# Performance work log

Hardware: AMD Instinct MI355X
Metric: run time of the kernel (lower is better)

Reference implementation:

```python
import jax, jax.numpy as jnp
import numpy as np


def setup_inputs() -> dict:
    key = jax.random.key(0)
    k1, k2, k3 = jax.random.split(key, 3)
    N, C, H, W, O = 4, 256, 64, 64, 256
    x = jax.random.normal(k1, (N, C, H, W), jnp.float32)
    # offset per forward signature: [N, H*W, 2*3*3]
    offset = jax.random.normal(k2, (N, H * W, 18), jnp.float32)
    # DeformConv weight [O, C, 3, 3], normal_init std=0.01, bias=False
    weight = jax.random.normal(k3, (O, C, 3, 3), jnp.float32) * 0.01
    return {"x": x, "offset": offset, "weight": weight}


def _deform_conv3x3(x, offset, weight):
    """Deformable conv v1: 3x3, stride 1, padding 1, dilation 1, no bias.
    x: [N,C,H,W]; offset: [N,HW,18] (permuted to [N,18,H,W] as in the module);
    weight: [O,C,3,3].
    """
    N, C, H, W = x.shape
    O = weight.shape[0]
    # module does offset.permute(0,2,1).reshape(N,-1,H,W) -> [N,18,H,W]
    off = offset.transpose(0, 2, 1).reshape(N, 9, 2, H, W)  # (dy,dx) per kernel pos
    dy, dx = off[:, :, 0], off[:, :, 1]                      # [N,9,H,W]

    # base 3x3 kernel offsets (padding=1 keeps the grid centered)
    ky = jnp.array([-1, -1, -1, 0, 0, 0, 1, 1, 1], x.dtype)
    kx = jnp.array([-1, 0, 1, -1, 0, 1, -1, 0, 1], x.dtype)
    hg = jnp.arange(H, dtype=x.dtype)[:, None]  # [H,1]
    wg = jnp.arange(W, dtype=x.dtype)[None, :]  # [1,W]
    py = hg[None, None] + ky[None, :, None, None] + dy  # [N,9,H,W] sample rows
    px = wg[None, None] + kx[None, :, None, None] + dx  # [N,9,H,W] sample cols

    y0 = jnp.floor(py)
    x0 = jnp.floor(px)
    wy = (py - y0)[:, None]  # [N,1,9,H,W]
    wx = (px - x0)[:, None]

    def gather(iy, ix):
        # zero-padded gather: out[n,c,k,h,w] = x[n,c,iy,ix] (0 if out of bounds)
        valid = (iy >= 0) & (iy < H) & (ix >= 0) & (ix < W)
        iyc = jnp.clip(iy, 0, H - 1).astype(jnp.int32)
        ixc = jnp.clip(ix, 0, W - 1).astype(jnp.int32)
        g = jax.vmap(lambda xn, yn, wn: xn[:, yn, wn])(x, iyc, ixc)  # [N,C,9,H,W]
        return g * valid[:, None].astype(x.dtype)

    v00 = gather(y0, x0)
    v01 = gather(y0, x0 + 1)
    v10 = gather(y0 + 1, x0)
    v11 = gather(y0 + 1, x0 + 1)
    # bilinear blend -> sampled columns [N,C,9,H,W]
    val = (v00 * (1 - wy) * (1 - wx) + v01 * (1 - wy) * wx
           + v10 * wy * (1 - wx) + v11 * wy * wx)
    # conv accumulate over channels and kernel positions
    return jnp.einsum('nckhw,ock->nohw', val, weight.reshape(O, C, 9))


def reference(x, offset, weight):
    return _deform_conv3x3(x, offset, weight)
```

## Files before the change

kernel.cpp:

```cpp
#include <hip/hip_runtime.h>
#include <hip/hip_fp16.h>

#define CC 256
#define OO 256
#define HH 64
#define WW 64
#define HWN 4096
#define MPB 64
#define NPB 128
#define VST 264

typedef _Float16 half8 __attribute__((ext_vector_type(8)));
typedef _Float16 half2v __attribute__((ext_vector_type(2)));
typedef float f32x4 __attribute__((ext_vector_type(4)));

__device__ __forceinline__ half2v u2h(unsigned u) {
  half2v h; __builtin_memcpy(&h, &u, 4); return h;
}
__device__ __forceinline__ unsigned h2u(half2v h) {
  unsigned u; __builtin_memcpy(&u, &h, 4); return u;
}
__device__ __forceinline__ unsigned short f2h(float f) {
  _Float16 h = (_Float16)f;
  unsigned short us; __builtin_memcpy(&us, &h, 2);
  return us;
}
__device__ __forceinline__ unsigned dupu(unsigned short us) {
  return ((unsigned)us << 16) | us;
}
__device__ __forceinline__ unsigned pk2(float a, float b) {
  half2v h = {(_Float16)a, (_Float16)b};
  return h2u(h);
}

__global__ __launch_bounds__(256) void prep_kernel(
    const float* __restrict__ x, const float* __restrict__ w,
    _Float16* __restrict__ xt, _Float16* __restrict__ wt) {
  const int bid = blockIdx.x;
  const int tid = threadIdx.x;
  if (bid < 1024) {
    __shared__ float tile[64][65];
    const int n  = bid >> 8;
    const int c0 = ((bid >> 6) & 3) * 64;
    const int s0 = (bid & 63) * 64;
    {
      int r  = tid >> 2;
      int sc = (tid & 3) * 16;
      const float* xp = x + ((size_t)(n * CC + c0 + r)) * HWN + s0 + sc;
      float4 va = *(const float4*)(xp);
      float4 vb = *(const float4*)(xp + 4);
      float4 vc = *(const float4*)(xp + 8);
      float4 vd = *(const float4*)(xp + 12);
      tile[sc + 0][r]  = va.x;  tile[sc + 1][r]  = va.y;
      tile[sc + 2][r]  = va.z;  tile[sc + 3][r]  = va.w;
      tile[sc + 4][r]  = vb.x;  tile[sc + 5][r]  = vb.y;
      tile[sc + 6][r]  = vb.z;  tile[sc + 7][r]  = vb.w;
      tile[sc + 8][r]  = vc.x;  tile[sc + 9][r]  = vc.y;
      tile[sc + 10][r] = vc.z;  tile[sc + 11][r] = vc.w;
      tile[sc + 12][r] = vd.x;  tile[sc + 13][r] = vd.y;
      tile[sc + 14][r] = vd.z;  tile[sc + 15][r] = vd.w;
    }
    __syncthreads();
    {
      int s  = tid >> 2;
      int cg = (tid & 3) * 16;
      uint4 u0, u1;
      u0.x = pk2(tile[s][cg + 0],  tile[s][cg + 1]);
      u0.y = pk2(tile[s][cg + 2],  tile[s][cg + 3]);
      u0.z = pk2(tile[s][cg + 4],  tile[s][cg + 5]);
      u0.w = pk2(tile[s][cg + 6],  tile[s][cg + 7]);
      u1.x = pk2(tile[s][cg + 8],  tile[s][cg + 9]);
      u1.y = pk2(tile[s][cg + 10], tile[s][cg + 11]);
      u1.z = pk2(tile[s][cg + 12], tile[s][cg + 13]);
      u1.w = pk2(tile[s][cg + 14], tile[s][cg + 15]);
      _Float16* op = xt + ((size_t)(n * HWN + s0 + s)) * CC + c0 + cg;
      *(uint4*)(op)     = u0;
      *(uint4*)(op + 8) = u1;
    }
  } else {
    __shared__ _Float16 wrow[9][264];
    const int o = bid - 1024;
    const float* wp = w + (size_t)o * (CC * 9);
    float v[9];
#pragma unroll
    for (int k = 0; k < 9; ++k) v[k] = wp[tid * 9 + k];
#pragma unroll
    for (int k = 0; k < 9; ++k) wrow[k][tid] = (_Float16)v[k];
    __syncthreads();
    for (int r = tid; r < 9 * 64; r += 256) {
      int k  = r >> 6;
      int c4 = (r & 63) * 4;
      *(uint2*)(wt + (size_t)k * (OO * CC) + (size_t)o * CC + c4) =
          *(const uint2*)(&wrow[k][c4]);
    }
  }
}

__global__ __launch_bounds__(256, 3) void deform_mfma_kernel(
    const _Float16* __restrict__ xt,
    const _Float16* __restrict__ wt,
    const float* __restrict__ off,
    float* __restrict__ out) {
  __shared__ __align__(16) _Float16 val_lds[MPB * VST];
  __shared__ ushort4 s_po[MPB * 9];
  __shared__ ushort4 s_pw[MPB * 9];

  const int tid  = threadIdx.x;
  const int lane = tid & 63;
  const int wv   = tid >> 6;
  const int n15  = lane & 15;
  const int quad = lane >> 4;

  const int bx    = blockIdx.x;
  const int nb    = (bx & 7) >> 1;
  const int hw0   = (bx >> 3) * MPB;
  const int obase = (bx & 1) * NPB;

  for (int e = tid; e < MPB * 9; e += 256) {
    int p = e / 9;
    int k = e - p * 9;
    int hw = hw0 + p;
    int h = hw >> 6, w = hw & 63;
    size_t ob = ((size_t)(nb * HWN + hw)) * 18 + 2 * k;
    float2 d = *(const float2*)(off + ob);
    float py = (float)(h + k / 3 - 1) + d.x;
    float px = (float)(w + k % 3 - 1) + d.y;
    float fy = floorf(py), fx = floorf(px);
    int iy = (int)fy, ix = (int)fx;
    float wy = py - fy, wx = px - fx;
    float my0 = ((unsigned)iy       < (unsigned)HH) ? 1.f : 0.f;
    float my1 = ((unsigned)(iy + 1) < (unsigned)HH) ? 1.f : 0.f;
    float mx0 = ((unsigned)ix       < (unsigned)WW) ? 1.f : 0.f;
    float mx1 = ((unsigned)(ix + 1) < (unsigned)WW) ? 1.f : 0.f;
    int iy0 = min(max(iy, 0), HH - 1), iy1 = min(max(iy + 1, 0), HH - 1);
    int ix0 = min(max(ix, 0), WW - 1), ix1 = min(max(ix + 1, 0), WW - 1);
    s_po[e] = make_ushort4((unsigned short)(iy0 * WW + ix0),
                           (unsigned short)(iy0 * WW + ix1),
                           (unsigned short)(iy1 * WW + ix0),
                           (unsigned short)(iy1 * WW + ix1));
    s_pw[e] = make_ushort4(f2h((1.f - wy) * (1.f - wx) * my0 * mx0),
                           f2h((1.f - wy) * wx         * my0 * mx1),
                           f2h(wy         * (1.f - wx) * my1 * mx0),
                           f2h(wy         * wx         * my1 * mx1));
  }

  f32x4 acc[4][2];
#pragma unroll
  for (int a = 0; a < 4; ++a)
#pragma unroll
    for (int b = 0; b < 2; ++b) acc[a][b] = (f32x4){0.f, 0.f, 0.f, 0.f};

  const _Float16* xb = xt + (size_t)nb * HWN * CC;
  const int j = lane & 31;
  const int ph = lane >> 5;

  for (int k = 0; k < 9; ++k) {
    __syncthreads();

    const _Float16* wb = wt + ((size_t)(k * OO + obase + wv * 32)) * CC;
    half8 bfr[8][2];
#pragma unroll
    for (int ks = 0; ks < 8; ++ks)
#pragma unroll
      for (int nt = 0; nt < 2; ++nt)
        bfr[ks][nt] = *(const half8*)(wb + (size_t)(nt * 16 + n15) * CC + ks * 32 + quad * 8);

#pragma unroll
    for (int i = 0; i < 8; ++i) {
      int p = i * 8 + wv * 2 + ph;
      int idx = p * 9 + k;
      ushort4 o4 = s_po[idx];
      ushort4 hw4 = s_pw[idx];
      half2v w00 = u2h(dupu(hw4.x)), w01 = u2h(dupu(hw4.y));
      half2v w10 = u2h(dupu(hw4.z)), w11 = u2h(dupu(hw4.w));
      const _Float16* cb = xb + (size_t)j * 8;
      uint4 v00 = *(const uint4*)(cb + (size_t)o4.x * CC);
      uint4 v01 = *(const uint4*)(cb + (size_t)o4.y * CC);
      uint4 v10 = *(const uint4*)(cb + (size_t)o4.z * CC);
      uint4 v11 = *(const uint4*)(cb + (size_t)o4.w * CC);
      uint4 r;
      r.x = h2u(u2h(v00.x) * w00 + u2h(v01.x) * w01 + u2h(v10.x) * w10 + u2h(v11.x) * w11);
      r.y = h2u(u2h(v00.y) * w00 + u2h(v01.y) * w01 + u2h(v10.y) * w10 + u2h(v11.y) * w11);
      r.z = h2u(u2h(v00.z) * w00 + u2h(v01.z) * w01 + u2h(v10.z) * w10 + u2h(v11.z) * w11);
      r.w = h2u(u2h(v00.w) * w00 + u2h(v01.w) * w01 + u2h(v10.w) * w10 + u2h(v11.w) * w11);
      *(uint4*)(val_lds + p * VST + j * 8) = r;
    }
    __syncthreads();

#pragma unroll
    for (int ks = 0; ks < 8; ++ks) {
      half8 afr[4];
#pragma unroll
      for (int mt = 0; mt < 4; ++mt)
        afr[mt] = *(const half8*)(val_lds + (mt * 16 + n15) * VST + ks * 32 + quad * 8);
#pragma unroll
      for (int mt = 0; mt < 4; ++mt)
#pragma unroll
        for (int nt = 0; nt < 2; ++nt)
          acc[mt][nt] = __builtin_amdgcn_mfma_f32_16x16x32_f16(
              afr[mt], bfr[ks][nt], acc[mt][nt], 0, 0, 0);
    }
  }

#pragma unroll
  for (int mt = 0; mt < 4; ++mt)
#pragma unroll
    for (int nt = 0; nt < 2; ++nt) {
      int o  = obase + wv * 32 + nt * 16 + n15;
      int px = hw0 + mt * 16 + quad * 4;
      *(f32x4*)(out + ((size_t)nb * OO + o) * HWN + px) = acc[mt][nt];
    }
}

extern "C" void kernel_launch(void* const* d_in, const int* in_sizes, int n_in,
                              void* d_out, int out_size, void* d_ws, size_t ws_size,
                              hipStream_t stream) {
  const float* x   = (const float*)d_in[0];
  const float* off = (const float*)d_in[1];
  const float* w   = (const float*)d_in[2];
  float* out = (float*)d_out;

  _Float16* wt = (_Float16*)d_ws;
  _Float16* xt = wt + 589824;

  prep_kernel<<<1024 + 256, 256, 0, stream>>>(x, w, xt, wt);
  deform_mfma_kernel<<<(4 * HWN / MPB) * (OO / NPB), 256, 0, stream>>>(xt, wt, off, out);
}
```

Baseline: 137.4 us.

## Double-buffer sampled columns to overlap bilinear gather with MFMA compute

Adds a second LDS buffer for the bilinearly sampled columns so that the gather for kernel position k+1 is interleaved with the MFMA accumulation for position k. One of the two barriers per iteration goes away, and weight fragments are now loaded per k-slice rather than all up front. In exchange LDS use doubles and launch bounds drop to 2 blocks per CU, which may reduce occupancy and latency hiding.

```diff
diff --git a/kernel.cpp b/kernel.cpp
--- a/kernel.cpp
+++ b/kernel.cpp
@@ -9,6 +9,7 @@
 #define MPB 64
 #define NPB 128
 #define VST 264
+#define VOFF (MPB * VST)
 
 typedef _Float16 half8 __attribute__((ext_vector_type(8)));
 typedef _Float16 half2v __attribute__((ext_vector_type(2)));
@@ -96,12 +97,12 @@
   }
 }
 
-__global__ __launch_bounds__(256, 3) void deform_mfma_kernel(
+__global__ __launch_bounds__(256, 2) void deform_mfma_kernel(
     const _Float16* __restrict__ xt,
     const _Float16* __restrict__ wt,
     const float* __restrict__ off,
     float* __restrict__ out) {
-  __shared__ __align__(16) _Float16 val_lds[MPB * VST];
+  __shared__ __align__(16) _Float16 val_lds[2 * VOFF];
   __shared__ ushort4 s_po[MPB * 9];
   __shared__ ushort4 s_pw[MPB * 9];
 
@@ -154,51 +155,74 @@
   const int j = lane & 31;
   const int ph = lane >> 5;
 
-  for (int k = 0; k < 9; ++k) {
+  auto sample_iter = [&](int kk, int bb, int i) {
+    int p = i * 8 + wv * 2 + ph;
+    int idx = p * 9 + kk;
+    ushort4 o4 = s_po[idx];
+    ushort4 hw4 = s_pw[idx];
+    half2v w00 = u2h(dupu(hw4.x)), w01 = u2h(dupu(hw4.y));
+    half2v w10 = u2h(dupu(hw4.z)), w11 = u2h(dupu(hw4.w));
+    const _Float16* cb = xb + (size_t)j * 8;
+    uint4 v00 = *(const uint4*)(cb + (size_t)o4.x * CC);
+    uint4 v01 = *(const uint4*)(cb + (size_t)o4.y * CC);
+    uint4 v10 = *(const uint4*)(cb + (size_t)o4.z * CC);
+    uint4 v11 = *(const uint4*)(cb + (size_t)o4.w * CC);
+    uint4 r;
+    r.x = h2u(u2h(v00.x) * w00 + u2h(v01.x) * w01 + u2h(v10.x) * w10 + u2h(v11.x) * w11);
+    r.y = h2u(u2h(v00.y) * w00 + u2h(v01.y) * w01 + u2h(v10.y) * w10 + u2h(v11.y) * w11);
+    r.z = h2u(u2h(v00.z) * w00 + u2h(v01.z) * w01 + u2h(v10.z) * w10 + u2h(v11.z) * w11);
+    r.w = h2u(u2h(v00.w) * w00 + u2h(v01.w) * w01 + u2h(v10.w) * w10 + u2h(v11.w) * w11);
+    *(uint4*)(val_lds + bb * VOFF + p * VST + j * 8) = r;
+  };
+
+  __syncthreads();
+#pragma unroll
+  for (int i = 0; i < 8; ++i) sample_iter(0, 0, i);
+
+  for (int k = 0; k < 8; ++k) {
     __syncthreads();
-
+    const int cur = k & 1;
+    const int nxt = cur ^ 1;
     const _Float16* wb = wt + ((size_t)(k * OO + obase + wv * 32)) * CC;
-    half8 bfr[8][2];
-#pragma unroll
-    for (int ks = 0; ks < 8; ++ks)
+#pragma unroll
+    for (int ks = 0; ks < 8; ++ks) {
+      sample_iter(k + 1, nxt, ks);
+      half8 bfr[2];
 #pragma unroll
       for (int nt = 0; nt < 2; ++nt)
-        bfr[ks][nt] = *(const half8*)(wb + (size_t)(nt * 16 + n15) * CC + ks * 32 + quad * 8);
-
-#pragma unroll
-    for (int i = 0; i < 8; ++i) {
-      int p = i * 8 + wv * 2 + ph;
-      int idx = p * 9 + k;
-      ushort4 o4 = s_po[idx];
-      ushort4 hw4 = s_pw[idx];
-      half2v w00 = u2h(dupu(hw4.x)), w01 = u2h(dupu(hw4.y));
-      half2v w10 = u2h(dupu(hw4.z)), w11 = u2h(dupu(hw4.w));
-      const _Float16* cb = xb + (size_t)j * 8;
-      uint4 v00 = *(const uint4*)(cb + (size_t)o4.x * CC);
-      uint4 v01 = *(const uint4*)(cb + (size_t)o4.y * CC);
-      uint4 v10 = *(const uint4*)(cb + (size_t)o4.z * CC);
-      uint4 v11 = *(const uint4*)(cb + (size_t)o4.w * CC);
-      uint4 r;
-      r.x = h2u(u2h(v00.x) * w00 + u2h(v01.x) * w01 + u2h(v10.x) * w10 + u2h(v11.x) * w11);
-      r.y = h2u(u2h(v00.y) * w00 + u2h(v01.y) * w01 + u2h(v10.y) * w10 + u2h(v11.y) * w11);
-      r.z = h2u(u2h(v00.z) * w00 + u2h(v01.z) * w01 + u2h(v10.z) * w10 + u2h(v11.z) * w11);
-      r.w = h2u(u2h(v00.w) * w00 + u2h(v01.w) * w01 + u2h(v10.w) * w10 + u2h(v11.w) * w11);
-      *(uint4*)(val_lds + p * VST + j * 8) = r;
-    }
-    __syncthreads();
-
-#pragma unroll
-    for (int ks = 0; ks < 8; ++ks) {
+        bfr[nt] = *(const half8*)(wb + (size_t)(nt * 16 + n15) * CC + ks * 32 + quad * 8);
       half8 afr[4];
 #pragma unroll
       for (int mt = 0; mt < 4; ++mt)
-        afr[mt] = *(const half8*)(val_lds + (mt * 16 + n15) * VST + ks * 32 + quad * 8);
+        afr[mt] = *(const half8*)(val_lds + cur * VOFF + (mt * 16 + n15) * VST + ks * 32 + quad * 8);
 #pragma unroll
       for (int mt = 0; mt < 4; ++mt)
 #pragma unroll
         for (int nt = 0; nt < 2; ++nt)
           acc[mt][nt] = __builtin_amdgcn_mfma_f32_16x16x32_f16(
-              afr[mt], bfr[ks][nt], acc[mt][nt], 0, 0, 0);
+              afr[mt], bfr[nt], acc[mt][nt], 0, 0, 0);
+    }
+  }
+
+  __syncthreads();
+  {
+    const _Float16* wb = wt + ((size_t)(8 * OO + obase + wv * 32)) * CC;
+#pragma unroll
+    for (int ks = 0; ks < 8; ++ks) {
+      half8 bfr[2];
+#pragma unroll
+      for (int nt = 0; nt < 2; ++nt)
+        bfr[nt] = *(const half8*)(wb + (size_t)(nt * 16 + n15) * CC + ks * 32 + quad * 8);
+      half8 afr[4];
+#pragma unroll
+      for (int mt = 0; mt < 4; ++mt)
+        afr[mt] = *(const half8*)(val_lds + (mt * 16 + n15) * VST + ks * 32 + quad * 8);
+#pragma unroll
+      for (int mt = 0; mt < 4; ++mt)
+#pragma unroll
+        for (int nt = 0; nt < 2; ++nt)
+          acc[mt][nt] = __builtin_amdgcn_mfma_f32_16x16x32_f16(
+              afr[mt], bfr[nt], acc[mt][nt], 0, 0, 0);
     }
   }
 
```

New measurement: 133.1 us. 3.1% less time.

## Split channel reduction across blocks with atomic accumulation instead of output split

Applied to the files above, without the earlier changes.

Each block now covers all 256 output channels for a quarter of the input channels (a split-K of 4) rather than half the outputs over all channels. Results are accumulated into an output zeroed by a memset, using float atomics. Bilinear gather work per block drops and is no longer duplicated across two output halves. Weight fragments are loaded per k-step instead of preloaded, and occupancy is raised to 4 waves per SIMD. The cost is atomic traffic on the full output, an extra memset, and a nondeterministic summation order.

```diff
diff --git a/kernel.cpp b/kernel.cpp
--- a/kernel.cpp
+++ b/kernel.cpp
@@ -7,8 +7,8 @@
 #define WW 64
 #define HWN 4096
 #define MPB 64
-#define NPB 128
-#define VST 264
+#define KQ  64
+#define VST 72
 
 typedef _Float16 half8 __attribute__((ext_vector_type(8)));
 typedef _Float16 half2v __attribute__((ext_vector_type(2)));
@@ -96,7 +96,7 @@
   }
 }
 
-__global__ __launch_bounds__(256, 3) void deform_mfma_kernel(
+__global__ __launch_bounds__(256, 4) void deform_mfma_kernel(
     const _Float16* __restrict__ xt,
     const _Float16* __restrict__ wt,
     const float* __restrict__ off,
@@ -112,9 +112,12 @@
   const int quad = lane >> 4;
 
   const int bx    = blockIdx.x;
-  const int nb    = (bx & 7) >> 1;
-  const int hw0   = (bx >> 3) * MPB;
-  const int obase = (bx & 1) * NPB;
+  const int xcd   = bx & 7;
+  const int local = bx >> 3;
+  const int nb    = xcd >> 1;
+  const int kq    = local & 3;
+  const int hw0   = (((xcd & 1) << 5) | (local >> 2)) * 64;
+  const int c0    = kq * KQ;
 
   for (int e = tid; e < MPB * 9; e += 256) {
     int p = e / 9;
@@ -144,30 +147,22 @@
                            f2h(wy         * wx         * my1 * mx1));
   }
 
-  f32x4 acc[4][2];
+  f32x4 acc[4][4];
 #pragma unroll
   for (int a = 0; a < 4; ++a)
 #pragma unroll
-    for (int b = 0; b < 2; ++b) acc[a][b] = (f32x4){0.f, 0.f, 0.f, 0.f};
-
-  const _Float16* xb = xt + (size_t)nb * HWN * CC;
-  const int j = lane & 31;
-  const int ph = lane >> 5;
+    for (int b = 0; b < 4; ++b) acc[a][b] = (f32x4){0.f, 0.f, 0.f, 0.f};
+
+  const _Float16* xb = xt + (size_t)nb * HWN * CC + c0;
+  const int j  = lane & 7;
+  const int pl = lane >> 3;
 
   for (int k = 0; k < 9; ++k) {
     __syncthreads();
 
-    const _Float16* wb = wt + ((size_t)(k * OO + obase + wv * 32)) * CC;
-    half8 bfr[8][2];
-#pragma unroll
-    for (int ks = 0; ks < 8; ++ks)
-#pragma unroll
-      for (int nt = 0; nt < 2; ++nt)
-        bfr[ks][nt] = *(const half8*)(wb + (size_t)(nt * 16 + n15) * CC + ks * 32 + quad * 8);
-
-#pragma unroll
-    for (int i = 0; i < 8; ++i) {
-      int p = i * 8 + wv * 2 + ph;
+#pragma unroll
+    for (int i = 0; i < 2; ++i) {
+      int p = i * 32 + wv * 8 + pl;
       int idx = p * 9 + k;
       ushort4 o4 = s_po[idx];
       ushort4 hw4 = s_pw[idx];
@@ -187,28 +182,36 @@
     }
     __syncthreads();
 
-#pragma unroll
-    for (int ks = 0; ks < 8; ++ks) {
-      half8 afr[4];
+    const _Float16* wb = wt + ((size_t)(k * OO + wv * 64)) * CC + c0;
+#pragma unroll
+    for (int ks = 0; ks < 2; ++ks) {
+      half8 afr[4], bfr[4];
 #pragma unroll
       for (int mt = 0; mt < 4; ++mt)
         afr[mt] = *(const half8*)(val_lds + (mt * 16 + n15) * VST + ks * 32 + quad * 8);
 #pragma unroll
+      for (int nt = 0; nt < 4; ++nt)
+        bfr[nt] = *(const half8*)(wb + (size_t)(nt * 16 + n15) * CC + ks * 32 + quad * 8);
+#pragma unroll
       for (int mt = 0; mt < 4; ++mt)
 #pragma unroll
-        for (int nt = 0; nt < 2; ++nt)
+        for (int nt = 0; nt < 4; ++nt)
           acc[mt][nt] = __builtin_amdgcn_mfma_f32_16x16x32_f16(
-              afr[mt], bfr[ks][nt], acc[mt][nt], 0, 0, 0);
+              afr[mt], bfr[nt], acc[mt][nt], 0, 0, 0);
     }
   }
 
 #pragma unroll
   for (int mt = 0; mt < 4; ++mt)
 #pragma unroll
-    for (int nt = 0; nt < 2; ++nt) {
-      int o  = obase + wv * 32 + nt * 16 + n15;
+    for (int nt = 0; nt < 4; ++nt) {
+      int o  = wv * 64 + nt * 16 + n15;
       int px = hw0 + mt * 16 + quad * 4;
-      *(f32x4*)(out + ((size_t)nb * OO + o) * HWN + px) = acc[mt][nt];
+      float* dst = out + ((size_t)nb * OO + o) * HWN + px;
+      atomicAdd(dst + 0, acc[mt][nt].x);
+      atomicAdd(dst + 1, acc[mt][nt].y);
+      atomicAdd(dst + 2, acc[mt][nt].z);
+      atomicAdd(dst + 3, acc[mt][nt].w);
     }
 }
 
@@ -223,6 +226,7 @@
   _Float16* wt = (_Float16*)d_ws;
   _Float16* xt = wt + 589824;
 
+  hipMemsetAsync(d_out, 0, (size_t)4 * OO * HWN * sizeof(float), stream);
   prep_kernel<<<1024 + 256, 256, 0, stream>>>(x, w, xt, wt);
-  deform_mfma_kernel<<<(4 * HWN / MPB) * (OO / NPB), 256, 0, stream>>>(xt, wt, off, out);
-}
+  deform_mfma_kernel<<<1024, 256, 0, stream>>>(xt, wt, off, out);
+}
```

After: 325.8 us. 137% more time.

## Cover all output channels per block and stage weights via double-buffered LDS

Applied to the files above, without the earlier changes.

Each block now processes 32 pixels for all 256 output channels with 512 threads, so the bilinear gather of sampled columns is no longer repeated for two output-channel halves. Weights are streamed into LDS in 32-channel slices with double buffering instead of being loaded per wave into registers. This removes duplicated gather work and register pressure from weight fragments. The cost is a barrier per K-slice and lower MFMA work per LDS read.

```diff
diff --git a/kernel.cpp b/kernel.cpp
--- a/kernel.cpp
+++ b/kernel.cpp
@@ -6,9 +6,10 @@
 #define HH 64
 #define WW 64
 #define HWN 4096
-#define MPB 64
-#define NPB 128
+#define MPB 32
 #define VST 264
+#define WST 44
+#define WBUF (256 * WST)
 
 typedef _Float16 half8 __attribute__((ext_vector_type(8)));
 typedef _Float16 half2v __attribute__((ext_vector_type(2)));
@@ -96,12 +97,13 @@
   }
 }
 
-__global__ __launch_bounds__(256, 3) void deform_mfma_kernel(
+__global__ __launch_bounds__(512, 4) void deform_mfma_kernel(
     const _Float16* __restrict__ xt,
     const _Float16* __restrict__ wt,
     const float* __restrict__ off,
     float* __restrict__ out) {
   __shared__ __align__(16) _Float16 val_lds[MPB * VST];
+  __shared__ __align__(16) _Float16 w_lds[2 * WBUF];
   __shared__ ushort4 s_po[MPB * 9];
   __shared__ ushort4 s_pw[MPB * 9];
 
@@ -111,12 +113,16 @@
   const int n15  = lane & 15;
   const int quad = lane >> 4;
 
-  const int bx    = blockIdx.x;
-  const int nb    = (bx & 7) >> 1;
-  const int hw0   = (bx >> 3) * MPB;
-  const int obase = (bx & 1) * NPB;
-
-  for (int e = tid; e < MPB * 9; e += 256) {
+  const int bx  = blockIdx.x;
+  const int xcd = bx & 7;
+  const int nb  = xcd >> 1;
+  const int hw0 = ((((xcd & 1) << 6) + (bx >> 3))) * MPB;
+
+  const int o0 = (wv & 3) * 64;
+  const int p0 = (wv >> 2) * 16;
+
+  if (tid < MPB * 9) {
+    int e = tid;
     int p = e / 9;
     int k = e - p * 9;
     int hw = hw0 + p;
@@ -144,30 +150,22 @@
                            f2h(wy         * wx         * my1 * mx1));
   }
 
-  f32x4 acc[4][2];
-#pragma unroll
-  for (int a = 0; a < 4; ++a)
-#pragma unroll
-    for (int b = 0; b < 2; ++b) acc[a][b] = (f32x4){0.f, 0.f, 0.f, 0.f};
+  f32x4 acc[4];
+#pragma unroll
+  for (int b = 0; b < 4; ++b) acc[b] = (f32x4){0.f, 0.f, 0.f, 0.f};
 
   const _Float16* xb = xt + (size_t)nb * HWN * CC;
-  const int j = lane & 31;
-  const int ph = lane >> 5;
+  const int j    = tid & 31;
+  const int slot = tid >> 5;
+  const int so   = tid >> 1;
+  const int sh   = tid & 1;
 
   for (int k = 0; k < 9; ++k) {
     __syncthreads();
 
-    const _Float16* wb = wt + ((size_t)(k * OO + obase + wv * 32)) * CC;
-    half8 bfr[8][2];
-#pragma unroll
-    for (int ks = 0; ks < 8; ++ks)
-#pragma unroll
-      for (int nt = 0; nt < 2; ++nt)
-        bfr[ks][nt] = *(const half8*)(wb + (size_t)(nt * 16 + n15) * CC + ks * 32 + quad * 8);
-
-#pragma unroll
-    for (int i = 0; i < 8; ++i) {
-      int p = i * 8 + wv * 2 + ph;
+#pragma unroll
+    for (int i = 0; i < 2; ++i) {
+      int p = i * 16 + slot;
       int idx = p * 9 + k;
       ushort4 o4 = s_po[idx];
       ushort4 hw4 = s_pw[idx];
@@ -185,31 +183,42 @@
       r.w = h2u(u2h(v00.w) * w00 + u2h(v01.w) * w01 + u2h(v10.w) * w10 + u2h(v11.w) * w11);
       *(uint4*)(val_lds + p * VST + j * 8) = r;
     }
+
+    {
+      const uint4* src = (const uint4*)(wt + ((size_t)(k * OO + so)) * CC + sh * 16);
+      uint4* dst = (uint4*)(w_lds + so * WST + sh * 16);
+      dst[0] = src[0];
+      dst[1] = src[1];
+    }
     __syncthreads();
 
 #pragma unroll
     for (int ks = 0; ks < 8; ++ks) {
-      half8 afr[4];
-#pragma unroll
-      for (int mt = 0; mt < 4; ++mt)
-        afr[mt] = *(const half8*)(val_lds + (mt * 16 + n15) * VST + ks * 32 + quad * 8);
-#pragma unroll
-      for (int mt = 0; mt < 4; ++mt)
-#pragma unroll
-        for (int nt = 0; nt < 2; ++nt)
-          acc[mt][nt] = __builtin_amdgcn_mfma_f32_16x16x32_f16(
-              afr[mt], bfr[ks][nt], acc[mt][nt], 0, 0, 0);
-    }
-  }
-
-#pragma unroll
-  for (int mt = 0; mt < 4; ++mt)
-#pragma unroll
-    for (int nt = 0; nt < 2; ++nt) {
-      int o  = obase + wv * 32 + nt * 16 + n15;
-      int px = hw0 + mt * 16 + quad * 4;
-      *(f32x4*)(out + ((size_t)nb * OO + o) * HWN + px) = acc[mt][nt];
-    }
+      const int cur = ks & 1;
+      if (ks < 7) {
+        const uint4* src = (const uint4*)(wt + ((size_t)(k * OO + so)) * CC + (ks + 1) * 32 + sh * 16);
+        uint4* dst = (uint4*)(w_lds + (cur ^ 1) * WBUF + so * WST + sh * 16);
+        dst[0] = src[0];
+        dst[1] = src[1];
+      }
+      half8 afr = *(const half8*)(val_lds + (p0 + n15) * VST + ks * 32 + quad * 8);
+      half8 bfr[4];
+#pragma unroll
+      for (int nt = 0; nt < 4; ++nt)
+        bfr[nt] = *(const half8*)(w_lds + cur * WBUF + (o0 + nt * 16 + n15) * WST + quad * 8);
+#pragma unroll
+      for (int nt = 0; nt < 4; ++nt)
+        acc[nt] = __builtin_amdgcn_mfma_f32_16x16x32_f16(afr, bfr[nt], acc[nt], 0, 0, 0);
+      if (ks < 7) __syncthreads();
+    }
+  }
+
+#pragma unroll
+  for (int nt = 0; nt < 4; ++nt) {
+    int o  = o0 + nt * 16 + n15;
+    int px = hw0 + p0 + quad * 4;
+    *(f32x4*)(out + ((size_t)nb * OO + o) * HWN + px) = acc[nt];
+  }
 }
 
 extern "C" void kernel_launch(void* const* d_in, const int* in_sizes, int n_in,
@@ -224,5 +233,5 @@
   _Float16* xt = wt + 589824;
 
   prep_kernel<<<1024 + 256, 256, 0, stream>>>(x, w, xt, wt);
-  deform_mfma_kernel<<<(4 * HWN / MPB) * (OO / NPB), 256, 0, stream>>>(xt, wt, off, out);
-}
+  deform_mfma_kernel<<<512, 512, 0, stream>>>(xt, wt, off, out);
+}
```

New measurement: 174.8 us. 27.2% more time.
